# Kernel optimization log

Hardware: AMD Instinct MI355X
Metric: run time of the kernel (lower is better)

Reference implementation:

```python
import jax, jax.numpy as jnp
import numpy as np

SCALE = 100.0  # sharp-softmax temperature from the torch module

def _build_tables():
    # ByteToNibbleFFN: W1 is identity(256) so it is mathematically a no-op; keep W2.
    W2_b2n = np.zeros((256, 32), np.float32)
    bb = np.arange(256)
    W2_b2n[bb, bb >> 4] = 1.0
    W2_b2n[bb, 16 + (bb & 15)] = 1.0
    # NibbleAddWithCarryFFN tables
    W1_add = np.zeros((34, 512), np.float32)
    W2_sum = np.zeros((512, 16), np.float32)
    W2_cout = np.zeros((512, 2), np.float32)
    for a in range(16):
        for b in range(16):
            for c in range(2):
                idx = a * 32 + b * 2 + c
                W1_add[a, idx] = 1.0
                W1_add[16 + b, idx] = 1.0
                W1_add[32 + c, idx] = 1.0
                t = a + b + c
                W2_sum[idx, t & 15] = 1.0
                W2_cout[idx, 1 if t > 15 else 0] = 1.0
    # NibbleToByteFFN tables
    W1_n2b = np.zeros((32, 256), np.float32)
    W2_n2b = np.zeros((256, 256), np.float32)
    for h in range(16):
        for l in range(16):
            addr = h * 16 + l
            W1_n2b[h, addr] = 1.0
            W1_n2b[16 + l, addr] = 1.0
            W2_n2b[addr, (h << 4) | l] = 1.0
    return tuple(jnp.asarray(t) for t in (W2_b2n, W1_add, W2_sum, W2_cout, W1_n2b, W2_n2b))

W2_B2N, W1_ADD, W2_SUM, W2_COUT, W1_N2B, W2_N2B = _build_tables()

def _b2n(x):
    # byte [.,256] -> (high [.,16], low [.,16]); W1=eye(256) omitted (identity)
    out = x @ W2_B2N
    return out[..., :16], out[..., 16:]

def _nib_add(a, b, cin):
    combined = jnp.concatenate([a, b, cin], axis=-1)           # [.,34]
    address = jax.nn.softmax(combined @ W1_ADD * SCALE, axis=-1)  # [.,512]
    return address @ W2_SUM, address @ W2_COUT

def _n2b(high, low):
    combined = jnp.concatenate([high, low], axis=-1)           # [.,32]
    address = jax.nn.softmax(combined @ W1_N2B * SCALE, axis=-1)  # [.,256]
    return address @ W2_N2B

def setup_inputs() -> dict:
    key = jax.random.key(0)
    k1, k2 = jax.random.split(key)
    B = 32768
    a = jax.random.uniform(k1, (B, 4, 256), dtype=jnp.float32)
    b = jax.random.uniform(k2, (B, 4, 256), dtype=jnp.float32)
    return {"a": a, "b": b}

def reference(a, b):
    # NeuralALU.add: ripple-carry add over 4 bytes, 2 nibble adds per byte
    B = a.shape[0]
    carry = jnp.zeros((B, 2), a.dtype).at[:, 0].set(1.0)  # carry_zero one-hot
    out_bytes = []
    for i in range(4):  # fixed structural loop over bytes (carry dependence)
        ah, al = _b2n(a[:, i])
        bh, bl = _b2n(b[:, i])
        sl, carry = _nib_add(al, bl, carry)
        sh, carry = _nib_add(ah, bh, carry)
        out_bytes.append(_n2b(sh, sl))
    return jnp.stack(out_bytes, axis=1)  # [B,4,256]
```

## Files before the change

kernel.cpp:

```cpp
#include <hip/hip_runtime.h>

#define NIB_SCALE 100.0f

template<int CTRL>
__device__ __forceinline__ float fdpp(float x) {
    return __int_as_float(__builtin_amdgcn_update_dpp(
        0, __float_as_int(x), CTRL, 0xF, 0xF, true));
}

__device__ __forceinline__ float rsum16d(float v) {
    v += fdpp<0x121>(v); v += fdpp<0x122>(v); v += fdpp<0x124>(v); v += fdpp<0x128>(v);
    return v;
}
__device__ __forceinline__ float rmax16d(float v) {
    v = fmaxf(v, fdpp<0x121>(v)); v = fmaxf(v, fdpp<0x122>(v));
    v = fmaxf(v, fdpp<0x124>(v)); v = fmaxf(v, fdpp<0x128>(v));
    return v;
}
__device__ __forceinline__ float scan16d(float v) {
    v += fdpp<0x111>(v); v += fdpp<0x112>(v); v += fdpp<0x114>(v); v += fdpp<0x118>(v);
    return v;
}
__device__ __forceinline__ float softmax16d(float v) {
    float m = rmax16d(v);
    float e = __expf(NIB_SCALE * (v - m));
    float s = rsum16d(e);
    return e / s;
}
__device__ __forceinline__ float sharp_sigmoid(float c) {
    return 1.0f / (1.0f + __expf(NIB_SCALE * (1.0f - 2.0f * c)));
}

#define GATHER_ROT(dst, src)            \
    dst[0]  = (src);                    \
    dst[1]  = fdpp<0x121>(src);         \
    dst[2]  = fdpp<0x122>(src);         \
    dst[3]  = fdpp<0x123>(src);         \
    dst[4]  = fdpp<0x124>(src);         \
    dst[5]  = fdpp<0x125>(src);         \
    dst[6]  = fdpp<0x126>(src);         \
    dst[7]  = fdpp<0x127>(src);         \
    dst[8]  = fdpp<0x128>(src);         \
    dst[9]  = fdpp<0x129>(src);         \
    dst[10] = fdpp<0x12A>(src);         \
    dst[11] = fdpp<0x12B>(src);         \
    dst[12] = fdpp<0x12C>(src);         \
    dst[13] = fdpp<0x12D>(src);         \
    dst[14] = fdpp<0x12E>(src);         \
    dst[15] = fdpp<0x12F>(src);

__global__ __launch_bounds__(256) void nalu_kernel(const float* __restrict__ A,
                                                   const float* __restrict__ B,
                                                   float* __restrict__ O,
                                                   int nrows) {
    __shared__ __align__(16) float sQL[16][16];
    __shared__ __align__(16) float sQH[16][16];
    __shared__ __align__(16) float sPSL[16][16];
    __shared__ __align__(16) float sPSH[16][16];
    __shared__ __align__(16) float sOV[4][4][4];

    const int tid = threadIdx.x;
    const int k = tid & 15;
    const int g = tid >> 4;
    const int b = g & 3;
    const int w = tid >> 6;
    const int row = blockIdx.x * 4 + w;
    if (row >= nrows) return;
    const long base = (long)row * 1024 + b * 256;

    const float* pa = A + base;
    const float* pb = B + base;

    float a0 = 0, a1 = 0, a2 = 0, a3 = 0, b0 = 0, b1 = 0, b2 = 0, b3 = 0;
    #pragma unroll
    for (int e = 0; e < 4; ++e) {
        a0 += pa[16 * e + k];        b0 += pb[16 * e + k];
        a1 += pa[16 * (e + 4) + k];  b1 += pb[16 * (e + 4) + k];
        a2 += pa[16 * (e + 8) + k];  b2 += pb[16 * (e + 8) + k];
        a3 += pa[16 * (e + 12) + k]; b3 += pb[16 * (e + 12) + k];
    }
    float al = (a0 + a1) + (a2 + a3);
    float bl = (b0 + b1) + (b2 + b3);
    const float4* pa4 = (const float4*)(pa + 16 * k);
    const float4* pb4 = (const float4*)(pb + 16 * k);
    float4 ra0 = pa4[0], ra1 = pa4[1], ra2 = pa4[2], ra3 = pa4[3];
    float4 rb0 = pb4[0], rb1 = pb4[1], rb2 = pb4[2], rb3 = pb4[3];
    float ah = ((ra0.x + ra0.y) + (ra0.z + ra0.w)) + ((ra1.x + ra1.y) + (ra1.z + ra1.w))
             + ((ra2.x + ra2.y) + (ra2.z + ra2.w)) + ((ra3.x + ra3.y) + (ra3.z + ra3.w));
    float bh = ((rb0.x + rb0.y) + (rb0.z + rb0.w)) + ((rb1.x + rb1.y) + (rb1.z + rb1.w))
             + ((rb2.x + rb2.y) + (rb2.z + rb2.w)) + ((rb3.x + rb3.y) + (rb3.z + rb3.w));

    float pal = softmax16d(al);
    float pbl = softmax16d(bl);
    float pah = softmax16d(ah);
    float pbh = softmax16d(bh);

    sQL[g][k] = pbl;
    sQH[g][k] = pbh;

    float mirl = fdpp<0x140>(pbl);
    float mirh = fdpp<0x140>(pbh);
    float T15l = scan16d(mirl);
    float T15h = scan16d(mirh);
    float ov15l = rsum16d(pal * T15l);
    float c15l  = rsum16d(pal * mirl);
    float ov15h = rsum16d(pah * T15h);
    float c15h  = rsum16d(pah * mirh);
    float ov16l = ov15l - c15l;
    float ov16h = ov15h - c15h;

    sOV[w][0][b] = ov16l;
    sOV[w][1][b] = ov15l;
    sOV[w][2][b] = ov16h;
    sOV[w][3][b] = ov15h;

    float QL[16], QH[16];
    *(float4*)&QL[0]  = *(const float4*)&sQL[g][0];
    *(float4*)&QL[4]  = *(const float4*)&sQL[g][4];
    *(float4*)&QL[8]  = *(const float4*)&sQL[g][8];
    *(float4*)&QL[12] = *(const float4*)&sQL[g][12];
    float GL[16];
    GATHER_ROT(GL, pal)
    float rl = 0.f;
    #pragma unroll
    for (int j = 0; j < 16; ++j) rl = fmaf(GL[j], QL[j], rl);

    *(float4*)&QH[0]  = *(const float4*)&sQH[g][0];
    *(float4*)&QH[4]  = *(const float4*)&sQH[g][4];
    *(float4*)&QH[8]  = *(const float4*)&sQH[g][8];
    *(float4*)&QH[12] = *(const float4*)&sQH[g][12];
    float GH[16];
    GATHER_ROT(GH, pah)
    float rh = 0.f;
    #pragma unroll
    for (int j = 0; j < 16; ++j) rh = fmaf(GH[j], QH[j], rh);

    float4 O16L = *(const float4*)&sOV[w][0][0];
    float4 O15L = *(const float4*)&sOV[w][1][0];
    float4 O16H = *(const float4*)&sOV[w][2][0];
    float4 O15H = *(const float4*)&sOV[w][3][0];

    float qc1_0 = sharp_sigmoid(O16L.x);
    float qc0_0 = 1.f - qc1_0;
    float pc1_1 = sharp_sigmoid(qc0_0 * O16H.x + qc1_0 * O15H.x);
    float pc0_1 = 1.f - pc1_1;
    float qc1_1 = sharp_sigmoid(pc0_1 * O16L.y + pc1_1 * O15L.y);
    float qc0_1 = 1.f - qc1_1;
    float pc1_2 = sharp_sigmoid(qc0_1 * O16H.y + qc1_1 * O15H.y);
    float pc0_2 = 1.f - pc1_2;
    float qc1_2 = sharp_sigmoid(pc0_2 * O16L.z + pc1_2 * O15L.z);
    float qc0_2 = 1.f - qc1_2;
    float pc1_3 = sharp_sigmoid(qc0_2 * O16H.z + qc1_2 * O15H.z);
    float pc0_3 = 1.f - pc1_3;
    float qc1_3 = sharp_sigmoid(pc0_3 * O16L.w + pc1_3 * O15L.w);
    float qc0_3 = 1.f - qc1_3;

    float pc0 = b == 0 ? 1.f   : b == 1 ? pc0_1 : b == 2 ? pc0_2 : pc0_3;
    float pc1 = b == 0 ? 0.f   : b == 1 ? pc1_1 : b == 2 ? pc1_2 : pc1_3;
    float qc0 = b == 0 ? qc0_0 : b == 1 ? qc0_1 : b == 2 ? qc0_2 : qc0_3;
    float qc1 = b == 0 ? qc1_0 : b == 1 ? qc1_1 : b == 2 ? qc1_2 : qc1_3;

    float slow  = pc0 * rl + pc1 * fdpp<0x121>(rl);
    float shigh = qc0 * rh + qc1 * fdpp<0x121>(rh);

    float psl = softmax16d(slow);
    float psh = softmax16d(shigh);
    sPSL[g][k] = psl;
    sPSH[g][k] = psh;

    float4 pslq = *(const float4*)&sPSL[g][4 * (k & 3)];
    float* po = O + base;
    #pragma unroll
    for (int c = 0; c < 4; ++c) {
        float hs = sPSH[g][4 * c + (k >> 2)];
        float4 o4 = make_float4(hs * pslq.x, hs * pslq.y, hs * pslq.z, hs * pslq.w);
        *(float4*)(po + 64 * c + 4 * k) = o4;
    }
}

extern "C" void kernel_launch(void* const* d_in, const int* in_sizes, int n_in,
                              void* d_out, int out_size, void* d_ws, size_t ws_size,
                              hipStream_t stream) {
    const float* A = (const float*)d_in[0];
    const float* B = (const float*)d_in[1];
    float* O = (float*)d_out;
    int nrows = in_sizes[0] / 1024;
    int grid = (nrows + 3) / 4;
    nalu_kernel<<<grid, 256, 0, stream>>>(A, B, O, nrows);
}
```

Baseline: 303.8 us.

## Use persistent waves with register prefetch and coalesced float4 nibble reductions

Switches to a persistent grid of 8192 waves, each looping over rows and prefetching the next row's A/B data into registers while computing the current one. Input loading now uses one coalesced set of float4 loads per operand, and both the high and low nibble sums are rebuilt from those registers with DPP, swizzle and bpermute cross-lane reductions. Before, each value was read twice with strided scalar loads. The goal is to halve input load traffic and hide memory latency, at the cost of more registers (launch bounds now request 6 blocks) and extra cross-lane shuffle work.

```diff
diff --git a/kernel.cpp b/kernel.cpp
--- a/kernel.cpp
+++ b/kernel.cpp
@@ -1,11 +1,18 @@
 #include <hip/hip_runtime.h>
 
 #define NIB_SCALE 100.0f
+#define NWAVES_TOTAL 8192
 
 template<int CTRL>
 __device__ __forceinline__ float fdpp(float x) {
     return __int_as_float(__builtin_amdgcn_update_dpp(
         0, __float_as_int(x), CTRL, 0xF, 0xF, true));
+}
+__device__ __forceinline__ float fswz_xor4(float x) {
+    return __int_as_float(__builtin_amdgcn_ds_swizzle(__float_as_int(x), 0x101F));
+}
+__device__ __forceinline__ float fbperm(int byteIdx, float v) {
+    return __int_as_float(__builtin_amdgcn_ds_bpermute(byteIdx, __float_as_int(v)));
 }
 
 __device__ __forceinline__ float rsum16d(float v) {
@@ -49,10 +56,10 @@
     dst[14] = fdpp<0x12E>(src);         \
     dst[15] = fdpp<0x12F>(src);
 
-__global__ __launch_bounds__(256) void nalu_kernel(const float* __restrict__ A,
-                                                   const float* __restrict__ B,
-                                                   float* __restrict__ O,
-                                                   int nrows) {
+__global__ __launch_bounds__(256, 6) void nalu_kernel(const float* __restrict__ A,
+                                                      const float* __restrict__ B,
+                                                      float* __restrict__ O,
+                                                      int nrows) {
     __shared__ __align__(16) float sQL[16][16];
     __shared__ __align__(16) float sQH[16][16];
     __shared__ __align__(16) float sPSL[16][16];
@@ -64,117 +71,154 @@
     const int g = tid >> 4;
     const int b = g & 3;
     const int w = tid >> 6;
-    const int row = blockIdx.x * 4 + w;
-    if (row >= nrows) return;
-    const long base = (long)row * 1024 + b * 256;
-
-    const float* pa = A + base;
-    const float* pb = B + base;
-
-    float a0 = 0, a1 = 0, a2 = 0, a3 = 0, b0 = 0, b1 = 0, b2 = 0, b3 = 0;
-    #pragma unroll
-    for (int e = 0; e < 4; ++e) {
-        a0 += pa[16 * e + k];        b0 += pb[16 * e + k];
-        a1 += pa[16 * (e + 4) + k];  b1 += pb[16 * (e + 4) + k];
-        a2 += pa[16 * (e + 8) + k];  b2 += pb[16 * (e + 8) + k];
-        a3 += pa[16 * (e + 12) + k]; b3 += pb[16 * (e + 12) + k];
+    const int lane64 = tid & 63;
+    const int bpermIdx = 4 * ((lane64 & 48) | ((k & 3) << 2) | (k >> 2));
+    const int wg = blockIdx.x * 4 + w;
+    const int RP = (nrows + NWAVES_TOTAL - 1) / NWAVES_TOTAL;
+
+    int row = wg;
+    float4 cA0, cA1, cA2, cA3, cB0, cB1, cB2, cB3;
+    if (row < nrows) {
+        const float4* pa4 = (const float4*)(A + (long)row * 1024 + b * 256);
+        const float4* pb4 = (const float4*)(B + (long)row * 1024 + b * 256);
+        cA0 = pa4[k]; cA1 = pa4[16 + k]; cA2 = pa4[32 + k]; cA3 = pa4[48 + k];
+        cB0 = pb4[k]; cB1 = pb4[16 + k]; cB2 = pb4[32 + k]; cB3 = pb4[48 + k];
     }
-    float al = (a0 + a1) + (a2 + a3);
-    float bl = (b0 + b1) + (b2 + b3);
-    const float4* pa4 = (const float4*)(pa + 16 * k);
-    const float4* pb4 = (const float4*)(pb + 16 * k);
-    float4 ra0 = pa4[0], ra1 = pa4[1], ra2 = pa4[2], ra3 = pa4[3];
-    float4 rb0 = pb4[0], rb1 = pb4[1], rb2 = pb4[2], rb3 = pb4[3];
-    float ah = ((ra0.x + ra0.y) + (ra0.z + ra0.w)) + ((ra1.x + ra1.y) + (ra1.z + ra1.w))
-             + ((ra2.x + ra2.y) + (ra2.z + ra2.w)) + ((ra3.x + ra3.y) + (ra3.z + ra3.w));
-    float bh = ((rb0.x + rb0.y) + (rb0.z + rb0.w)) + ((rb1.x + rb1.y) + (rb1.z + rb1.w))
-             + ((rb2.x + rb2.y) + (rb2.z + rb2.w)) + ((rb3.x + rb3.y) + (rb3.z + rb3.w));
-
-    float pal = softmax16d(al);
-    float pbl = softmax16d(bl);
-    float pah = softmax16d(ah);
-    float pbh = softmax16d(bh);
-
-    sQL[g][k] = pbl;
-    sQH[g][k] = pbh;
-
-    float mirl = fdpp<0x140>(pbl);
-    float mirh = fdpp<0x140>(pbh);
-    float T15l = scan16d(mirl);
-    float T15h = scan16d(mirh);
-    float ov15l = rsum16d(pal * T15l);
-    float c15l  = rsum16d(pal * mirl);
-    float ov15h = rsum16d(pah * T15h);
-    float c15h  = rsum16d(pah * mirh);
-    float ov16l = ov15l - c15l;
-    float ov16h = ov15h - c15h;
-
-    sOV[w][0][b] = ov16l;
-    sOV[w][1][b] = ov15l;
-    sOV[w][2][b] = ov16h;
-    sOV[w][3][b] = ov15h;
-
-    float QL[16], QH[16];
-    *(float4*)&QL[0]  = *(const float4*)&sQL[g][0];
-    *(float4*)&QL[4]  = *(const float4*)&sQL[g][4];
-    *(float4*)&QL[8]  = *(const float4*)&sQL[g][8];
-    *(float4*)&QL[12] = *(const float4*)&sQL[g][12];
-    float GL[16];
-    GATHER_ROT(GL, pal)
-    float rl = 0.f;
-    #pragma unroll
-    for (int j = 0; j < 16; ++j) rl = fmaf(GL[j], QL[j], rl);
-
-    *(float4*)&QH[0]  = *(const float4*)&sQH[g][0];
-    *(float4*)&QH[4]  = *(const float4*)&sQH[g][4];
-    *(float4*)&QH[8]  = *(const float4*)&sQH[g][8];
-    *(float4*)&QH[12] = *(const float4*)&sQH[g][12];
-    float GH[16];
-    GATHER_ROT(GH, pah)
-    float rh = 0.f;
-    #pragma unroll
-    for (int j = 0; j < 16; ++j) rh = fmaf(GH[j], QH[j], rh);
-
-    float4 O16L = *(const float4*)&sOV[w][0][0];
-    float4 O15L = *(const float4*)&sOV[w][1][0];
-    float4 O16H = *(const float4*)&sOV[w][2][0];
-    float4 O15H = *(const float4*)&sOV[w][3][0];
-
-    float qc1_0 = sharp_sigmoid(O16L.x);
-    float qc0_0 = 1.f - qc1_0;
-    float pc1_1 = sharp_sigmoid(qc0_0 * O16H.x + qc1_0 * O15H.x);
-    float pc0_1 = 1.f - pc1_1;
-    float qc1_1 = sharp_sigmoid(pc0_1 * O16L.y + pc1_1 * O15L.y);
-    float qc0_1 = 1.f - qc1_1;
-    float pc1_2 = sharp_sigmoid(qc0_1 * O16H.y + qc1_1 * O15H.y);
-    float pc0_2 = 1.f - pc1_2;
-    float qc1_2 = sharp_sigmoid(pc0_2 * O16L.z + pc1_2 * O15L.z);
-    float qc0_2 = 1.f - qc1_2;
-    float pc1_3 = sharp_sigmoid(qc0_2 * O16H.z + qc1_2 * O15H.z);
-    float pc0_3 = 1.f - pc1_3;
-    float qc1_3 = sharp_sigmoid(pc0_3 * O16L.w + pc1_3 * O15L.w);
-    float qc0_3 = 1.f - qc1_3;
-
-    float pc0 = b == 0 ? 1.f   : b == 1 ? pc0_1 : b == 2 ? pc0_2 : pc0_3;
-    float pc1 = b == 0 ? 0.f   : b == 1 ? pc1_1 : b == 2 ? pc1_2 : pc1_3;
-    float qc0 = b == 0 ? qc0_0 : b == 1 ? qc0_1 : b == 2 ? qc0_2 : qc0_3;
-    float qc1 = b == 0 ? qc1_0 : b == 1 ? qc1_1 : b == 2 ? qc1_2 : qc1_3;
-
-    float slow  = pc0 * rl + pc1 * fdpp<0x121>(rl);
-    float shigh = qc0 * rh + qc1 * fdpp<0x121>(rh);
-
-    float psl = softmax16d(slow);
-    float psh = softmax16d(shigh);
-    sPSL[g][k] = psl;
-    sPSH[g][k] = psh;
-
-    float4 pslq = *(const float4*)&sPSL[g][4 * (k & 3)];
-    float* po = O + base;
-    #pragma unroll
-    for (int c = 0; c < 4; ++c) {
-        float hs = sPSH[g][4 * c + (k >> 2)];
-        float4 o4 = make_float4(hs * pslq.x, hs * pslq.y, hs * pslq.z, hs * pslq.w);
-        *(float4*)(po + 64 * c + 4 * k) = o4;
+
+    for (int it = 0; it < RP; ++it) {
+        const int nxtRow = row + NWAVES_TOTAL;
+
+        float ahj[4], bhj[4];
+        {
+            float s;
+            s = (cA0.x + cA0.y) + (cA0.z + cA0.w); s += fdpp<0xB1>(s); s += fdpp<0x4E>(s); ahj[0] = s;
+            s = (cA1.x + cA1.y) + (cA1.z + cA1.w); s += fdpp<0xB1>(s); s += fdpp<0x4E>(s); ahj[1] = s;
+            s = (cA2.x + cA2.y) + (cA2.z + cA2.w); s += fdpp<0xB1>(s); s += fdpp<0x4E>(s); ahj[2] = s;
+            s = (cA3.x + cA3.y) + (cA3.z + cA3.w); s += fdpp<0xB1>(s); s += fdpp<0x4E>(s); ahj[3] = s;
+            s = (cB0.x + cB0.y) + (cB0.z + cB0.w); s += fdpp<0xB1>(s); s += fdpp<0x4E>(s); bhj[0] = s;
+            s = (cB1.x + cB1.y) + (cB1.z + cB1.w); s += fdpp<0xB1>(s); s += fdpp<0x4E>(s); bhj[1] = s;
+            s = (cB2.x + cB2.y) + (cB2.z + cB2.w); s += fdpp<0xB1>(s); s += fdpp<0x4E>(s); bhj[2] = s;
+            s = (cB3.x + cB3.y) + (cB3.z + cB3.w); s += fdpp<0xB1>(s); s += fdpp<0x4E>(s); bhj[3] = s;
+        }
+        float ali[4], bli[4];
+        {
+            float s;
+            s = (cA0.x + cA1.x) + (cA2.x + cA3.x); s += fswz_xor4(s); s += fdpp<0x128>(s); ali[0] = s;
+            s = (cA0.y + cA1.y) + (cA2.y + cA3.y); s += fswz_xor4(s); s += fdpp<0x128>(s); ali[1] = s;
+            s = (cA0.z + cA1.z) + (cA2.z + cA3.z); s += fswz_xor4(s); s += fdpp<0x128>(s); ali[2] = s;
+            s = (cA0.w + cA1.w) + (cA2.w + cA3.w); s += fswz_xor4(s); s += fdpp<0x128>(s); ali[3] = s;
+            s = (cB0.x + cB1.x) + (cB2.x + cB3.x); s += fswz_xor4(s); s += fdpp<0x128>(s); bli[0] = s;
+            s = (cB0.y + cB1.y) + (cB2.y + cB3.y); s += fswz_xor4(s); s += fdpp<0x128>(s); bli[1] = s;
+            s = (cB0.z + cB1.z) + (cB2.z + cB3.z); s += fswz_xor4(s); s += fdpp<0x128>(s); bli[2] = s;
+            s = (cB0.w + cB1.w) + (cB2.w + cB3.w); s += fswz_xor4(s); s += fdpp<0x128>(s); bli[3] = s;
+        }
+        float t0, t1;
+        t0 = (k & 4) ? ali[1] : ali[0]; t1 = (k & 4) ? ali[3] : ali[2];
+        float al = fbperm(bpermIdx, (k & 8) ? t1 : t0);
+        t0 = (k & 4) ? bli[1] : bli[0]; t1 = (k & 4) ? bli[3] : bli[2];
+        float bl = fbperm(bpermIdx, (k & 8) ? t1 : t0);
+        t0 = (k & 1) ? ahj[1] : ahj[0]; t1 = (k & 1) ? ahj[3] : ahj[2];
+        float ah = fbperm(bpermIdx, (k & 2) ? t1 : t0);
+        t0 = (k & 1) ? bhj[1] : bhj[0]; t1 = (k & 1) ? bhj[3] : bhj[2];
+        float bh = fbperm(bpermIdx, (k & 2) ? t1 : t0);
+
+        const bool vn = (it + 1 < RP) && (nxtRow < nrows);
+        if (vn) {
+            const float4* pa4 = (const float4*)(A + (long)nxtRow * 1024 + b * 256);
+            const float4* pb4 = (const float4*)(B + (long)nxtRow * 1024 + b * 256);
+            cA0 = pa4[k]; cA1 = pa4[16 + k]; cA2 = pa4[32 + k]; cA3 = pa4[48 + k];
+            cB0 = pb4[k]; cB1 = pb4[16 + k]; cB2 = pb4[32 + k]; cB3 = pb4[48 + k];
+        }
+
+        float pal = softmax16d(al);
+        float pbl = softmax16d(bl);
+        float pah = softmax16d(ah);
+        float pbh = softmax16d(bh);
+
+        sQL[g][k] = pbl;
+        sQH[g][k] = pbh;
+
+        float mirl = fdpp<0x140>(pbl);
+        float mirh = fdpp<0x140>(pbh);
+        float T15l = scan16d(mirl);
+        float T15h = scan16d(mirh);
+        float ov15l = rsum16d(pal * T15l);
+        float c15l  = rsum16d(pal * mirl);
+        float ov15h = rsum16d(pah * T15h);
+        float c15h  = rsum16d(pah * mirh);
+        float ov16l = ov15l - c15l;
+        float ov16h = ov15h - c15h;
+
+        sOV[w][0][b] = ov16l;
+        sOV[w][1][b] = ov15l;
+        sOV[w][2][b] = ov16h;
+        sOV[w][3][b] = ov15h;
+
+        float QL[16], QH[16];
+        *(float4*)&QL[0]  = *(const float4*)&sQL[g][0];
+        *(float4*)&QL[4]  = *(const float4*)&sQL[g][4];
+        *(float4*)&QL[8]  = *(const float4*)&sQL[g][8];
+        *(float4*)&QL[12] = *(const float4*)&sQL[g][12];
+        float GL[16];
+        GATHER_ROT(GL, pal)
+        float rl = 0.f;
+        #pragma unroll
+        for (int j = 0; j < 16; ++j) rl = fmaf(GL[j], QL[j], rl);
+
+        *(float4*)&QH[0]  = *(const float4*)&sQH[g][0];
+        *(float4*)&QH[4]  = *(const float4*)&sQH[g][4];
+        *(float4*)&QH[8]  = *(const float4*)&sQH[g][8];
+        *(float4*)&QH[12] = *(const float4*)&sQH[g][12];
+        float GH[16];
+        GATHER_ROT(GH, pah)
+        float rh = 0.f;
+        #pragma unroll
+        for (int j = 0; j < 16; ++j) rh = fmaf(GH[j], QH[j], rh);
+
+        float4 O16L = *(const float4*)&sOV[w][0][0];
+        float4 O15L = *(const float4*)&sOV[w][1][0];
+        float4 O16H = *(const float4*)&sOV[w][2][0];
+        float4 O15H = *(const float4*)&sOV[w][3][0];
+
+        float qc1_0 = sharp_sigmoid(O16L.x);
+        float qc0_0 = 1.f - qc1_0;
+        float pc1_1 = sharp_sigmoid(qc0_0 * O16H.x + qc1_0 * O15H.x);
+        float pc0_1 = 1.f - pc1_1;
+        float qc1_1 = sharp_sigmoid(pc0_1 * O16L.y + pc1_1 * O15L.y);
+        float qc0_1 = 1.f - qc1_1;
+        float pc1_2 = sharp_sigmoid(qc0_1 * O16H.y + qc1_1 * O15H.y);
+        float pc0_2 = 1.f - pc1_2;
+        float qc1_2 = sharp_sigmoid(pc0_2 * O16L.z + pc1_2 * O15L.z);
+        float qc0_2 = 1.f - qc1_2;
+        float pc1_3 = sharp_sigmoid(qc0_2 * O16H.z + qc1_2 * O15H.z);
+        float pc0_3 = 1.f - pc1_3;
+        float qc1_3 = sharp_sigmoid(pc0_3 * O16L.w + pc1_3 * O15L.w);
+        float qc0_3 = 1.f - qc1_3;
+
+        float pc0 = b == 0 ? 1.f   : b == 1 ? pc0_1 : b == 2 ? pc0_2 : pc0_3;
+        float pc1 = b == 0 ? 0.f   : b == 1 ? pc1_1 : b == 2 ? pc1_2 : pc1_3;
+        float qc0 = b == 0 ? qc0_0 : b == 1 ? qc0_1 : b == 2 ? qc0_2 : qc0_3;
+        float qc1 = b == 0 ? qc1_0 : b == 1 ? qc1_1 : b == 2 ? qc1_2 : qc1_3;
+
+        float slow  = pc0 * rl + pc1 * fdpp<0x121>(rl);
+        float shigh = qc0 * rh + qc1 * fdpp<0x121>(rh);
+
+        float psl = softmax16d(slow);
+        float psh = softmax16d(shigh);
+        sPSL[g][k] = psl;
+        sPSH[g][k] = psh;
+
+        float4 pslq = *(const float4*)&sPSL[g][4 * (k & 3)];
+        if (row < nrows) {
+            float* po = O + (long)row * 1024 + b * 256;
+            #pragma unroll
+            for (int c = 0; c < 4; ++c) {
+                float hs = sPSH[g][4 * c + (k >> 2)];
+                float4 o4 = make_float4(hs * pslq.x, hs * pslq.y, hs * pslq.z, hs * pslq.w);
+                *(float4*)(po + 64 * c + 4 * k) = o4;
+            }
+        }
+        row = nxtRow;
     }
 }
 
@@ -185,6 +229,5 @@
     const float* B = (const float*)d_in[1];
     float* O = (float*)d_out;
     int nrows = in_sizes[0] / 1024;
-    int grid = (nrows + 3) / 4;
-    nalu_kernel<<<grid, 256, 0, stream>>>(A, B, O, nrows);
-}
+    nalu_kernel<<<NWAVES_TOTAL / 4, 256, 0, stream>>>(A, B, O, nrows);
+}
```

New measurement: 355.5 us. 17.0% more time.
